# Optimization experiments

Hardware: AMD Instinct MI355X
Metric: run time of the kernel (lower is better)

Reference implementation:

```python
import jax, jax.numpy as jnp
import numpy as np

GRID_SIZE = 4
ORDER = 3
NUM_BASIS = GRID_SIZE + ORDER  # 7
KNOTS = jnp.linspace(-1.0, 1.0, NUM_BASIS + ORDER + 1)  # 11 knots


def _normalise(x):
    # eval-mode with uninitialized running stats: use batch min/max
    min_val = x.min(axis=0)
    max_val = x.max(axis=0)
    width = jnp.maximum(max_val - min_val, 0.01)
    centre = 0.5 * (max_val + min_val)
    scaled = (x - centre) / (0.5 * width)
    return jnp.clip(scaled, -2.0, 2.0)


def _bspline_basis(x):
    # x: (B, I) -> basis: (B, I, NUM_BASIS), de Boor recursion vectorized over i
    xe = x[..., None]  # (B, I, 1)
    idx = jnp.arange(NUM_BASIS)
    left, right = KNOTS[idx], KNOTS[idx + 1]
    basis = ((xe >= left) & (xe < right)).astype(x.dtype)
    last = jnp.where(xe[..., 0] == KNOTS[NUM_BASIS], 1.0, basis[..., -1])
    basis = basis.at[..., -1].set(last)
    for k in range(1, ORDER + 1):
        d1 = KNOTS[idx + k] - KNOTS[idx]
        d2 = KNOTS[idx + k + 1] - KNOTS[idx + 1]
        b_next = jnp.concatenate([basis[..., 1:], jnp.zeros_like(basis[..., :1])], axis=-1)
        t1 = jnp.where(d1 > 0, (xe - KNOTS[idx]) / jnp.where(d1 > 0, d1, 1.0), 0.0) * basis
        t2 = jnp.where(d2 > 0, (KNOTS[idx + k + 1] - xe) / jnp.where(d2 > 0, d2, 1.0), 0.0) * b_next
        basis = t1 + t2
    return basis


def setup_inputs() -> dict:
    key = jax.random.key(0)
    k1, k2, k3 = jax.random.split(key, 3)
    B, I, O = 8192, 256, 256
    x = jax.random.normal(k1, (B, I), dtype=jnp.float32)
    # xavier-uniform base_weight
    bound = float(np.sqrt(6.0 / (I + O)))
    base_weight = jax.random.uniform(k2, (O, I), minval=-bound, maxval=bound, dtype=jnp.float32)
    spline_weight = jnp.ones((O, I), dtype=jnp.float32)
    spline_coeff = 0.001 * jax.random.normal(k3, (O, I, NUM_BASIS), dtype=jnp.float32)
    bias = jnp.zeros((O,), dtype=jnp.float32)
    return {"x": x, "base_weight": base_weight, "spline_weight": spline_weight,
            "spline_coeff": spline_coeff, "bias": bias}


def reference(x, base_weight, spline_weight, spline_coeff, bias):
    x_norm = _normalise(x)                          # (B, I)
    basis = _bspline_basis(x_norm)                  # (B, I, M)
    silu_x = x_norm * jax.nn.sigmoid(x_norm)        # (B, I)
    base_out = silu_x @ base_weight.T               # sum_i silu_i * W_oi -> (B, O)
    coeff_scaled = spline_coeff * spline_weight[..., None]  # (O, I, M)
    spline_out = jnp.einsum('bim,oim->bo', basis, coeff_scaled)
    return base_out + spline_out + bias[None, :]
```

## Files before the change

kernel.cpp:

```cpp
#include <hip/hip_runtime.h>
#include <hip/hip_bf16.h>
#include <stdint.h>

#define B_SZ 8192
#define I_SZ 256
#define O_SZ 256
#define KDIM 2048
#define BMB 128
#define BNB 64
#define NPART 128

typedef __bf16 bf16x8 __attribute__((ext_vector_type(8)));
typedef float f32x4 __attribute__((ext_vector_type(4)));

__global__ __launch_bounds__(256) void minmax_partial(
    const float* __restrict__ x, float* __restrict__ pmin,
    float* __restrict__ pmax) {
  const int cg = threadIdx.x & 63;
  const int rs = threadIdx.x >> 6;
  const int r0 = blockIdx.x * 64;
  const float* p = x + (size_t)(r0 + rs) * I_SZ + cg * 4;
  float4 mn = {1e30f, 1e30f, 1e30f, 1e30f};
  float4 mx = {-1e30f, -1e30f, -1e30f, -1e30f};
#pragma unroll
  for (int k = 0; k < 16; ++k) {
    const float4 v = *reinterpret_cast<const float4*>(p + (size_t)k * 4 * I_SZ);
    mn.x = fminf(mn.x, v.x); mn.y = fminf(mn.y, v.y);
    mn.z = fminf(mn.z, v.z); mn.w = fminf(mn.w, v.w);
    mx.x = fmaxf(mx.x, v.x); mx.y = fmaxf(mx.y, v.y);
    mx.z = fmaxf(mx.z, v.z); mx.w = fmaxf(mx.w, v.w);
  }
  __shared__ float rmn[4][I_SZ], rmx[4][I_SZ];
  *reinterpret_cast<float4*>(&rmn[rs][cg * 4]) = mn;
  *reinterpret_cast<float4*>(&rmx[rs][cg * 4]) = mx;
  __syncthreads();
  if (threadIdx.x < 64) {
    float4 a, b;
    const int c0 = threadIdx.x * 4;
    a.x = fminf(fminf(rmn[0][c0+0], rmn[1][c0+0]), fminf(rmn[2][c0+0], rmn[3][c0+0]));
    a.y = fminf(fminf(rmn[0][c0+1], rmn[1][c0+1]), fminf(rmn[2][c0+1], rmn[3][c0+1]));
    a.z = fminf(fminf(rmn[0][c0+2], rmn[1][c0+2]), fminf(rmn[2][c0+2], rmn[3][c0+2]));
    a.w = fminf(fminf(rmn[0][c0+3], rmn[1][c0+3]), fminf(rmn[2][c0+3], rmn[3][c0+3]));
    b.x = fmaxf(fmaxf(rmx[0][c0+0], rmx[1][c0+0]), fmaxf(rmx[2][c0+0], rmx[3][c0+0]));
    b.y = fmaxf(fmaxf(rmx[0][c0+1], rmx[1][c0+1]), fmaxf(rmx[2][c0+1], rmx[3][c0+1]));
    b.z = fmaxf(fmaxf(rmx[0][c0+2], rmx[1][c0+2]), fmaxf(rmx[2][c0+2], rmx[3][c0+2]));
    b.w = fmaxf(fmaxf(rmx[0][c0+3], rmx[1][c0+3]), fmaxf(rmx[2][c0+3], rmx[3][c0+3]));
    *reinterpret_cast<float4*>(&pmin[blockIdx.x * I_SZ + c0]) = a;
    *reinterpret_cast<float4*>(&pmax[blockIdx.x * I_SZ + c0]) = b;
  }
}

__global__ void pack_W(const float* __restrict__ bw,
                       const float* __restrict__ sw,
                       const float* __restrict__ coeff,
                       __hip_bfloat16* __restrict__ W,
                       const float* __restrict__ pmin,
                       const float* __restrict__ pmax,
                       float* __restrict__ cenrhw) {
  const int idx = blockIdx.x * blockDim.x + threadIdx.x;
  const int i = idx & (I_SZ - 1);
  const int o = idx >> 8;
  const float s = sw[idx];
  union { __hip_bfloat16 h[8]; float4 f4; } u;
#pragma unroll
  for (int m = 0; m < 7; ++m)
    u.h[m] = __float2bfloat16(coeff[(size_t)idx * 7 + m] * s);
  u.h[7] = __float2bfloat16(bw[idx]);
  const size_t off = (size_t)o * KDIM + (size_t)((i ^ (o & 7)) << 3);
  *reinterpret_cast<float4*>(&W[off]) = u.f4;

  if (blockIdx.x == 0) {
    const int c = threadIdx.x;
    float mn = 1e30f, mx = -1e30f;
#pragma unroll 8
    for (int p = 0; p < NPART; ++p) {
      mn = fminf(mn, pmin[p * I_SZ + c]);
      mx = fmaxf(mx, pmax[p * I_SZ + c]);
    }
    const float width = fmaxf(mx - mn, 0.01f);
    const float rhw = 2.0f / width;
    cenrhw[2 * c]     = rhw;
    cenrhw[2 * c + 1] = -0.5f * (mx + mn) * rhw;
  }
}

__device__ __forceinline__ void async16(const __hip_bfloat16* g, __hip_bfloat16* l) {
  __builtin_amdgcn_global_load_lds(
      (const __attribute__((address_space(1))) void*)g,
      (__attribute__((address_space(3))) void*)l, 16, 0, 0);
}

__device__ __forceinline__ uint32_t bfc(float f) {
  union { __hip_bfloat16 b; unsigned short s; } c;
  c.b = __float2bfloat16(f);
  return (uint32_t)c.s;
}

__device__ __forceinline__ bf16x8 evalOne(float xv, float2 s2) {
  const float xn = __builtin_fmaf(xv, s2.x, s2.y);
  const float sp = __builtin_fmaf(xn, 5.0f, 5.0f);
  const float c6 = fminf(fmaxf(floorf(sp), 0.0f), 6.0f);
  const int ci = (int)c6;
  const float u = sp - c6;
  const float zm = (sp > 7.0f) ? 0.0f : (1.0f / 6.0f);
  const float u2 = u * u, u3 = u2 * u, t1 = 1.0f - u;
  const float q3 = u3 * zm;
  const float q0 = (t1 * t1) * (t1 * zm);
  float h2 = __builtin_fmaf(-3.0f, u, 3.0f);
  h2 = __builtin_fmaf(h2, u, 3.0f);
  h2 = __builtin_fmaf(h2, u, 1.0f);
  float h1 = __builtin_fmaf(3.0f, u, -6.0f);
  h1 = __builtin_fmaf(h1, u2, 4.0f);
  const float q2v = h2 * zm, q1v = h1 * zm;
  const float silu = xn * __builtin_amdgcn_rcpf(1.0f + __expf(-xn));
  const uint64_t D = (uint64_t)(bfc(q0) | (bfc(q1v) << 16)) |
                     ((uint64_t)(bfc(q2v) | (bfc(q3) << 16)) << 32);
  const int tt = ci * 16 - 48;
  const uint64_t ls = D << (tt & 63);
  const uint64_t rs = D >> ((-tt) & 63);
  uint64_t lo = (tt >= 0) ? ls : rs;
  uint64_t hi = (tt >= 0) ? ((D >> ((63 - tt) & 63)) >> 1) : 0ull;
  hi = (hi & 0x0000FFFFFFFFFFFFull) | ((uint64_t)bfc(silu) << 48);
  union { uint32_t w[4]; bf16x8 v; } r;
  r.w[0] = (uint32_t)lo; r.w[1] = (uint32_t)(lo >> 32);
  r.w[2] = (uint32_t)hi; r.w[3] = (uint32_t)(hi >> 32);
  return r.v;
}

__global__ __launch_bounds__(256) void gemm_fused(
    const float* __restrict__ x, const __hip_bfloat16* __restrict__ W,
    const float* __restrict__ cenrhw, const float* __restrict__ bias,
    float* __restrict__ out) {
  __shared__ __align__(16) __hip_bfloat16 Wlds[BNB][1024];
  __shared__ float2 scl[I_SZ];

  const int t = threadIdx.x;
  const int lane = t & 63;
  const int wave = t >> 6;
  const int fr = lane & 15, fk = lane >> 4;

  const int bid = blockIdx.x;
  const int swz = (bid & 7) * 32 + (bid >> 3);
  const int bm = swz >> 2, bn = swz & 3;
  const int r0 = bm * BMB, c0 = bn * BNB;

  scl[t] = reinterpret_cast<const float2*>(cenrhw)[t];

  const __hip_bfloat16* gw = W + (size_t)(c0 + (t >> 7)) * KDIM + (t & 127) * 8;
  auto stageW = [&](int h) {
    const __hip_bfloat16* g = gw + h * 1024;
    __hip_bfloat16* l = &Wlds[0][0] + (size_t)t * 8;
#pragma unroll
    for (int q = 0; q < 32; ++q)
      async16(g + (size_t)2 * q * KDIM, l + (size_t)2048 * q);
  };

  const float* xq = x + (size_t)(r0 + wave * 32 + fr) * I_SZ + fk;

  f32x4 acc[2][4] = {{{0,0,0,0},{0,0,0,0},{0,0,0,0},{0,0,0,0}},
                     {{0,0,0,0},{0,0,0,0},{0,0,0,0},{0,0,0,0}}};

  stageW(0);
  float xc0[4], xc1[4], xn0[4], xn1[4];
#pragma unroll
  for (int s2 = 0; s2 < 4; ++s2) {
    xc0[s2] = xq[4 * s2];
    xc1[s2] = xq[16 * I_SZ + 4 * s2];
  }
  __syncthreads();

#pragma unroll 1
  for (int h = 0; h < 2; ++h) {
#pragma unroll 1
    for (int g = 0; g < 8; ++g) {
      const int gn = h * 8 + g + 1;
      if (gn < 16) {
        const int off = gn * 16;
#pragma unroll
        for (int s2 = 0; s2 < 4; ++s2) {
          xn0[s2] = xq[off + 4 * s2];
          xn1[s2] = xq[16 * I_SZ + off + 4 * s2];
        }
      }
#pragma unroll
      for (int s2 = 0; s2 < 4; ++s2) {
        const int gs = g * 4 + s2;
        const int f = h * 128 + gs * 4 + fk;
        const float2 s2c = scl[f];
        const bf16x8 a0 = evalOne(xc0[s2], s2c);
        const bf16x8 a1 = evalOne(xc1[s2], s2c);
        const int cp = gs * 4 + fk;
        const int grp = cp & ~7, low = cp & 7;
        bf16x8 bg[4];
#pragma unroll
        for (int n = 0; n < 4; ++n) {
          const int row = n * 16 + fr;
          const int cidx = grp | (low ^ (row & 7));
          bg[n] = *reinterpret_cast<const bf16x8*>(&Wlds[row][cidx * 8]);
        }
#pragma unroll
        for (int n = 0; n < 4; ++n) {
          acc[0][n] = __builtin_amdgcn_mfma_f32_16x16x32_bf16(a0, bg[n], acc[0][n], 0, 0, 0);
          acc[1][n] = __builtin_amdgcn_mfma_f32_16x16x32_bf16(a1, bg[n], acc[1][n], 0, 0, 0);
        }
      }
#pragma unroll
      for (int s2 = 0; s2 < 4; ++s2) { xc0[s2] = xn0[s2]; xc1[s2] = xn1[s2]; }
    }
    if (h == 0) {
      __syncthreads();
      stageW(1);
      __syncthreads();
    }
  }

#pragma unroll
  for (int m = 0; m < 2; ++m)
#pragma unroll
    for (int n = 0; n < 4; ++n) {
      const int col = c0 + n * 16 + fr;
      const float bc = bias[col];
#pragma unroll
      for (int r = 0; r < 4; ++r) {
        const int row = r0 + wave * 32 + m * 16 + fk * 4 + r;
        out[(size_t)row * O_SZ + col] = acc[m][n][r] + bc;
      }
    }
}

extern "C" void kernel_launch(void* const* d_in, const int* in_sizes, int n_in,
                              void* d_out, int out_size, void* d_ws, size_t ws_size,
                              hipStream_t stream) {
  const float* x     = (const float*)d_in[0];
  const float* bw    = (const float*)d_in[1];
  const float* sw    = (const float*)d_in[2];
  const float* coeff = (const float*)d_in[3];
  const float* bias  = (const float*)d_in[4];
  float* out = (float*)d_out;

  char* ws = (char*)d_ws;
  __hip_bfloat16* Wbuf = (__hip_bfloat16*)ws;
  float* pmin   = (float*)(ws + (size_t)O_SZ * KDIM * 2);
  float* pmax   = pmin + NPART * I_SZ;
  float* cenrhw = pmax + NPART * I_SZ;

  minmax_partial<<<NPART, 256, 0, stream>>>(x, pmin, pmax);
  pack_W<<<(O_SZ * I_SZ) / 256, 256, 0, stream>>>(bw, sw, coeff, Wbuf,
                                                  pmin, pmax, cenrhw);
  gemm_fused<<<(B_SZ / BMB) * (O_SZ / BNB), 256, 0, stream>>>(x, Wbuf, cenrhw,
                                                              bias, out);
}
```

Before: 44.52 us.

## Split GEMM K dimension across two wave groups and fuse min/max finalize

Doubles the GEMM block to 512 threads, with two groups of four waves each covering half of the K (input feature) range. The partial accumulators are then reduced through LDS before the epilogue adds bias and writes the output. The final min/max reduction over the partial buffers moves from one block of pack_W into every GEMM block. This adds intra-block parallelism and removes the serial tail from pack_W, at the cost of each of the 256 GEMM blocks redundantly reading 256 KB of partials plus an extra LDS reduction and extra barriers.

Result: slower. 58.68 us (+31.8%).

```diff
diff --git a/kernel.cpp b/kernel.cpp
--- a/kernel.cpp
+++ b/kernel.cpp
@@ -53,10 +53,7 @@
 __global__ void pack_W(const float* __restrict__ bw,
                        const float* __restrict__ sw,
                        const float* __restrict__ coeff,
-                       __hip_bfloat16* __restrict__ W,
-                       const float* __restrict__ pmin,
-                       const float* __restrict__ pmax,
-                       float* __restrict__ cenrhw) {
+                       __hip_bfloat16* __restrict__ W) {
   const int idx = blockIdx.x * blockDim.x + threadIdx.x;
   const int i = idx & (I_SZ - 1);
   const int o = idx >> 8;
@@ -68,20 +65,6 @@
   u.h[7] = __float2bfloat16(bw[idx]);
   const size_t off = (size_t)o * KDIM + (size_t)((i ^ (o & 7)) << 3);
   *reinterpret_cast<float4*>(&W[off]) = u.f4;
-
-  if (blockIdx.x == 0) {
-    const int c = threadIdx.x;
-    float mn = 1e30f, mx = -1e30f;
-#pragma unroll 8
-    for (int p = 0; p < NPART; ++p) {
-      mn = fminf(mn, pmin[p * I_SZ + c]);
-      mx = fmaxf(mx, pmax[p * I_SZ + c]);
-    }
-    const float width = fmaxf(mx - mn, 0.01f);
-    const float rhw = 2.0f / width;
-    cenrhw[2 * c]     = rhw;
-    cenrhw[2 * c + 1] = -0.5f * (mx + mn) * rhw;
-  }
 }
 
 __device__ __forceinline__ void async16(const __hip_bfloat16* g, __hip_bfloat16* l) {
@@ -127,16 +110,18 @@
   return r.v;
 }
 
-__global__ __launch_bounds__(256) void gemm_fused(
+__global__ __launch_bounds__(512, 2) void gemm_fused(
     const float* __restrict__ x, const __hip_bfloat16* __restrict__ W,
-    const float* __restrict__ cenrhw, const float* __restrict__ bias,
-    float* __restrict__ out) {
-  __shared__ __align__(16) __hip_bfloat16 Wlds[BNB][1024];
+    const float* __restrict__ pmin, const float* __restrict__ pmax,
+    const float* __restrict__ bias, float* __restrict__ out) {
+  __shared__ __align__(16) __hip_bfloat16 Wlds[2][64][512];
   __shared__ float2 scl[I_SZ];
 
   const int t = threadIdx.x;
   const int lane = t & 63;
   const int wave = t >> 6;
+  const int wr = wave & 3;
+  const int kh = wave >> 2;
   const int fr = lane & 15, fk = lane >> 4;
 
   const int bid = blockIdx.x;
@@ -144,59 +129,82 @@
   const int bm = swz >> 2, bn = swz & 3;
   const int r0 = bm * BMB, c0 = bn * BNB;
 
-  scl[t] = reinterpret_cast<const float2*>(cenrhw)[t];
-
-  const __hip_bfloat16* gw = W + (size_t)(c0 + (t >> 7)) * KDIM + (t & 127) * 8;
-  auto stageW = [&](int h) {
-    const __hip_bfloat16* g = gw + h * 1024;
-    __hip_bfloat16* l = &Wlds[0][0] + (size_t)t * 8;
-#pragma unroll
-    for (int q = 0; q < 32; ++q)
-      async16(g + (size_t)2 * q * KDIM, l + (size_t)2048 * q);
+  auto stageW = [&](int ph) {
+#pragma unroll
+    for (int c = 0; c < 16; ++c) {
+      const int idx = wave * 16 + c;
+      const int row = idx & 63, rg = idx >> 6;
+      async16(W + (size_t)(c0 + row) * KDIM + rg * 1024 + ph * 512 + lane * 8,
+              &Wlds[rg][row][0]);
+    }
   };
 
-  const float* xq = x + (size_t)(r0 + wave * 32 + fr) * I_SZ + fk;
+  stageW(0);
+
+  {
+    const int col = t & 255;
+    if (t < 256) {
+      float v = 1e30f;
+#pragma unroll 8
+      for (int p = 0; p < NPART; ++p) v = fminf(v, pmin[p * I_SZ + col]);
+      scl[col].x = v;
+    } else {
+      float v = -1e30f;
+#pragma unroll 8
+      for (int p = 0; p < NPART; ++p) v = fmaxf(v, pmax[p * I_SZ + col]);
+      scl[col].y = v;
+    }
+  }
+
+  const float* xq = x + (size_t)(r0 + wr * 32 + fr) * I_SZ + fk;
+  const int fb0 = kh * 128;
+  float xc[8], xn[8];
+#pragma unroll
+  for (int s = 0; s < 4; ++s) {
+    xc[s]     = xq[fb0 + 4 * s];
+    xc[4 + s] = xq[16 * I_SZ + fb0 + 4 * s];
+  }
+
+  __syncthreads();
+  if (t < 256) {
+    const float mn = scl[t].x, mx = scl[t].y;
+    const float w = fmaxf(mx - mn, 0.01f);
+    const float rhw = 2.0f / w;
+    scl[t] = make_float2(rhw, -0.5f * (mx + mn) * rhw);
+  }
+  __syncthreads();
 
   f32x4 acc[2][4] = {{{0,0,0,0},{0,0,0,0},{0,0,0,0},{0,0,0,0}},
                      {{0,0,0,0},{0,0,0,0},{0,0,0,0},{0,0,0,0}}};
 
-  stageW(0);
-  float xc0[4], xc1[4], xn0[4], xn1[4];
-#pragma unroll
-  for (int s2 = 0; s2 < 4; ++s2) {
-    xc0[s2] = xq[4 * s2];
-    xc1[s2] = xq[16 * I_SZ + 4 * s2];
-  }
-  __syncthreads();
-
 #pragma unroll 1
-  for (int h = 0; h < 2; ++h) {
+  for (int ph = 0; ph < 2; ++ph) {
+    const int fb = fb0 + ph * 64;
 #pragma unroll 1
-    for (int g = 0; g < 8; ++g) {
-      const int gn = h * 8 + g + 1;
-      if (gn < 16) {
-        const int off = gn * 16;
-#pragma unroll
-        for (int s2 = 0; s2 < 4; ++s2) {
-          xn0[s2] = xq[off + 4 * s2];
-          xn1[s2] = xq[16 * I_SZ + off + 4 * s2];
-        }
-      }
-#pragma unroll
-      for (int s2 = 0; s2 < 4; ++s2) {
-        const int gs = g * 4 + s2;
-        const int f = h * 128 + gs * 4 + fk;
-        const float2 s2c = scl[f];
-        const bf16x8 a0 = evalOne(xc0[s2], s2c);
-        const bf16x8 a1 = evalOne(xc1[s2], s2c);
-        const int cp = gs * 4 + fk;
-        const int grp = cp & ~7, low = cp & 7;
+    for (int g = 0; g < 4; ++g) {
+      if (!(ph == 1 && g == 3)) {
+        const int nfb  = (g == 3) ? fb0 + 64 : fb;
+        const int noff = (g == 3) ? 0 : (g + 1) * 16;
+#pragma unroll
+        for (int s = 0; s < 4; ++s) {
+          xn[s]     = xq[nfb + noff + 4 * s];
+          xn[4 + s] = xq[16 * I_SZ + nfb + noff + 4 * s];
+        }
+      }
+#pragma unroll
+      for (int s = 0; s < 4; ++s) {
+        const int ksp = g * 4 + s;
+        const float2 sc = scl[fb + ksp * 4 + fk];
+        const bf16x8 a0 = evalOne(xc[s], sc);
+        const bf16x8 a1 = evalOne(xc[4 + s], sc);
+        const int u = ksp * 4 + fk;
+        const int grp = u & ~7, low = u & 7;
         bf16x8 bg[4];
 #pragma unroll
         for (int n = 0; n < 4; ++n) {
           const int row = n * 16 + fr;
           const int cidx = grp | (low ^ (row & 7));
-          bg[n] = *reinterpret_cast<const bf16x8*>(&Wlds[row][cidx * 8]);
+          bg[n] = *reinterpret_cast<const bf16x8*>(&Wlds[kh][row][cidx * 8]);
         }
 #pragma unroll
         for (int n = 0; n < 4; ++n) {
@@ -205,27 +213,44 @@
         }
       }
 #pragma unroll
-      for (int s2 = 0; s2 < 4; ++s2) { xc0[s2] = xn0[s2]; xc1[s2] = xn1[s2]; }
-    }
-    if (h == 0) {
+      for (int j = 0; j < 8; ++j) xc[j] = xn[j];
+    }
+    if (ph == 0) {
       __syncthreads();
       stageW(1);
       __syncthreads();
     }
   }
 
-#pragma unroll
-  for (int m = 0; m < 2; ++m)
-#pragma unroll
-    for (int n = 0; n < 4; ++n) {
-      const int col = c0 + n * 16 + fr;
-      const float bc = bias[col];
-#pragma unroll
-      for (int r = 0; r < 4; ++r) {
-        const int row = r0 + wave * 32 + m * 16 + fk * 4 + r;
-        out[(size_t)row * O_SZ + col] = acc[m][n][r] + bc;
-      }
-    }
+  __syncthreads();
+  float* rbuf = reinterpret_cast<float*>(&Wlds[0][0][0]);
+  float* pb = rbuf + wr * 2048 + lane * 32;
+  if (kh == 1) {
+#pragma unroll
+    for (int m = 0; m < 2; ++m)
+#pragma unroll
+      for (int n = 0; n < 4; ++n) {
+        const int slot = ((m * 4 + n) + lane) & 7;
+        *reinterpret_cast<f32x4*>(&pb[slot * 4]) = acc[m][n];
+      }
+  }
+  __syncthreads();
+  if (kh == 0) {
+#pragma unroll
+    for (int m = 0; m < 2; ++m)
+#pragma unroll
+      for (int n = 0; n < 4; ++n) {
+        const int slot = ((m * 4 + n) + lane) & 7;
+        const f32x4 v = *reinterpret_cast<const f32x4*>(&pb[slot * 4]);
+        const int col = c0 + n * 16 + fr;
+        const float bc = bias[col];
+#pragma unroll
+        for (int r = 0; r < 4; ++r) {
+          const int row = r0 + wr * 32 + m * 16 + fk * 4 + r;
+          out[(size_t)row * O_SZ + col] = acc[m][n][r] + v[r] + bc;
+        }
+      }
+  }
 }
 
 extern "C" void kernel_launch(void* const* d_in, const int* in_sizes, int n_in,
@@ -240,13 +265,11 @@
 
   char* ws = (char*)d_ws;
   __hip_bfloat16* Wbuf = (__hip_bfloat16*)ws;
-  float* pmin   = (float*)(ws + (size_t)O_SZ * KDIM * 2);
-  float* pmax   = pmin + NPART * I_SZ;
-  float* cenrhw = pmax + NPART * I_SZ;
+  float* pmin = (float*)(ws + (size_t)O_SZ * KDIM * 2);
+  float* pmax = pmin + NPART * I_SZ;
 
   minmax_partial<<<NPART, 256, 0, stream>>>(x, pmin, pmax);
-  pack_W<<<(O_SZ * I_SZ) / 256, 256, 0, stream>>>(bw, sw, coeff, Wbuf,
-                                                  pmin, pmax, cenrhw);
-  gemm_fused<<<(B_SZ / BMB) * (O_SZ / BNB), 256, 0, stream>>>(x, Wbuf, cenrhw,
-                                                              bias, out);
-}
+  pack_W<<<(O_SZ * I_SZ) / 256, 256, 0, stream>>>(bw, sw, coeff, Wbuf);
+  gemm_fused<<<(B_SZ / BMB) * (O_SZ / BNB), 512, 0, stream>>>(x, Wbuf, pmin,
+                                                              pmax, bias, out);
+}
```
